# Kernel optimization log

Hardware: AMD Instinct MI355X
Metric: run time of the kernel (lower is better)

## Reference

```python
import jax, jax.numpy as jnp
import numpy as np


def setup_inputs() -> dict:
    key = jax.random.key(0)
    k_x, k_g, k_fc, k_pj = jax.random.split(key, 4)
    B, T, C, H, E = 4, 2048, 1024, 2048, 8
    n_layer = 12
    x = jax.random.normal(k_x, (B, T, C), dtype=jnp.float32)
    w_gate = 0.02 * jax.random.normal(k_g, (C, E), dtype=jnp.float32)
    w_fc = 0.02 * jax.random.normal(k_fc, (C, H, E), dtype=jnp.float32)
    w_proj = (0.02 * (2 * n_layer) ** -0.5) * jax.random.normal(k_pj, (H, C, E), dtype=jnp.float32)
    return {"x": x, "w_gate": w_gate, "w_fc": w_fc, "w_proj": w_proj, "top_k": 2}


def reference(x, w_gate, w_fc, w_proj, top_k):
    # x: (B,T,C); w_gate: (C,E); w_fc: (C,H,E); w_proj: (H,C,E)
    E = w_gate.shape[-1]
    gate = jnp.einsum('btc,ce->bte', x, w_gate)                  # gating logits
    top_vals, top_idx = jax.lax.top_k(gate, top_k)               # (B,T,K) — raw logits used as combine weights (as in source)
    # Per-expert combine weight: sum_k top_val_k * onehot(idx_k) — zero for unselected experts.
    # This is mathematically identical to gathering the K expert weight slices per token
    # (the source's gather+einsum) but avoids the (B,T,C,H,K) weight blowup.
    onehot = jax.nn.one_hot(top_idx, E, dtype=x.dtype)           # (B,T,K,E)
    w_e = jnp.einsum('btk,btke->bte', top_vals, onehot)          # (B,T,E)
    h = jax.nn.silu(jnp.einsum('btc,che->bthe', x, w_fc))        # (B,T,H,E)
    o = jnp.einsum('bthe,bte,hce->btc', h, w_e, w_proj)          # weighted expert combine
    return o
```

## Files before the change

kernel.cpp:

```cpp
#include <hip/hip_runtime.h>
#include <hip/hip_bf16.h>


#define NTOK 8192
#define CD   1024
#define HD   2048
#define NE   8
#define NSLOT 16384
#define MTILES 32

typedef short  short4_t  __attribute__((ext_vector_type(4)));
typedef short  short8_t  __attribute__((ext_vector_type(8)));
typedef __bf16 bf16x8_t  __attribute__((ext_vector_type(8)));
typedef float  f32x4_t   __attribute__((ext_vector_type(4)));

struct FragArg {
  short8_t v;
  __device__ operator short8_t() const { return v; }
  __device__ operator bf16x8_t() const { return __builtin_bit_cast(bf16x8_t, v); }
};

static __device__ __forceinline__ float b2f(unsigned short u) {
  union { float f; unsigned int i; } w; w.i = ((unsigned int)u) << 16; return w.f;
}
static __device__ __forceinline__ unsigned short f2b(float f) {
  unsigned int u = __float_as_uint(f);
  u += 0x7fffu + ((u >> 16) & 1u);
  return (unsigned short)(u >> 16);
}
static __device__ __forceinline__ void gl2lds16(const void* g, void* l) {
  __builtin_amdgcn_global_load_lds((__attribute__((address_space(1))) void*)g,
                                   (__attribute__((address_space(3))) void*)l,
                                   16, 0, 0);
}
static __device__ __forceinline__ int swz(int row, int kc) {
  return row * 4 + (kc ^ ((row >> 1) & 3));
}

__global__ __launch_bounds__(256) void gate_kernel(
    const float* __restrict__ x, const float* __restrict__ wg,
    unsigned short* __restrict__ xb,
    int* __restrict__ tok_e, float* __restrict__ tok_v)
{
  int wv = threadIdx.x >> 6, lane = threadIdx.x & 63;
  int tk = blockIdx.x * 4 + wv;
  const float* xr = x + (size_t)tk * CD;
  unsigned short* xbr = xb + (size_t)tk * CD;
  float acc[NE] = {0, 0, 0, 0, 0, 0, 0, 0};
  #pragma unroll
  for (int jj = 0; jj < 4; ++jj) {
    int c0 = (lane + 64 * jj) * 4;
    float4 xv = *(const float4*)(xr + c0);
    short4_t ob;
    ob[0] = (short)f2b(xv.x); ob[1] = (short)f2b(xv.y);
    ob[2] = (short)f2b(xv.z); ob[3] = (short)f2b(xv.w);
    *(short4_t*)(xbr + c0) = ob;
    #pragma unroll
    for (int j = 0; j < 4; ++j) {
      float xf = (j == 0) ? xv.x : (j == 1) ? xv.y : (j == 2) ? xv.z : xv.w;
      const float* wr = wg + (size_t)(c0 + j) * NE;
      float4 w0 = *(const float4*)wr;
      float4 w1 = *(const float4*)(wr + 4);
      acc[0] += xf * w0.x; acc[1] += xf * w0.y;
      acc[2] += xf * w0.z; acc[3] += xf * w0.w;
      acc[4] += xf * w1.x; acc[5] += xf * w1.y;
      acc[6] += xf * w1.z; acc[7] += xf * w1.w;
    }
  }
  #pragma unroll
  for (int off = 32; off >= 1; off >>= 1)
    #pragma unroll
    for (int e = 0; e < NE; ++e) acc[e] += __shfl_down(acc[e], off, 64);
  if (lane == 0) {
    float v1 = -3.0e38f, v2 = -3.0e38f; int i1 = 0, i2 = 1;
    #pragma unroll
    for (int e = 0; e < NE; ++e) {
      float g = acc[e];
      if (g > v1) { v2 = v1; i2 = i1; v1 = g; i1 = e; }
      else if (g > v2) { v2 = g; i2 = e; }
    }
    tok_e[tk * 2] = i1; tok_e[tk * 2 + 1] = i2;
    tok_v[tk * 2] = v1; tok_v[tk * 2 + 1] = v2;
  }
}

__global__ __launch_bounds__(256) void router_kernel(
    const int* __restrict__ tok_e, const float* __restrict__ tok_v,
    int* __restrict__ g_counts, int* __restrict__ g_base,
    int* __restrict__ bucket_tok, float* __restrict__ bucket_v,
    int* __restrict__ slot_of)
{
  __shared__ int cnts[NE][256];
  __shared__ int bas[NE], tot[NE];
  int t = threadIdx.x;
  int local[NE] = {0, 0, 0, 0, 0, 0, 0, 0};
  for (int i = 0; i < 64; ++i) local[tok_e[t * 64 + i]]++;
  #pragma unroll
  for (int e = 0; e < NE; ++e) cnts[e][t] = local[e];
  __syncthreads();
  int lane = t & 63, wv = t >> 6;
  for (int e = wv; e < NE; e += 4) {
    int carry = 0;
    #pragma unroll
    for (int c = 0; c < 4; ++c) {
      int v = cnts[e][c * 64 + lane];
      int incl = v;
      #pragma unroll
      for (int off = 1; off < 64; off <<= 1) {
        int n = __shfl_up(incl, off, 64);
        if (lane >= off) incl += n;
      }
      cnts[e][c * 64 + lane] = incl - v + carry;
      carry += __shfl(incl, 63, 64);
    }
    if (lane == 0) tot[e] = carry;
  }
  __syncthreads();
  if (t == 0) { int o = 0; for (int e = 0; e < NE; ++e) { bas[e] = o; o += tot[e]; } }
  __syncthreads();
  if (t < NE) { g_counts[t] = tot[t]; g_base[t] = bas[t]; }
  for (int i = 0; i < 64; ++i) {
    int s = t * 64 + i;
    int e = tok_e[s];
    int sl = bas[e] + cnts[e][t];
    cnts[e][t]++;
    bucket_tok[sl] = s >> 1;
    bucket_v[sl]   = tok_v[s];
    slot_of[s]     = sl;
  }
}

__global__ __launch_bounds__(256) void pack_kernel(
    const float* __restrict__ wfc, const float* __restrict__ wpj,
    unsigned short* __restrict__ wfcp, unsigned short* __restrict__ wpjp)
{
  __shared__ __align__(16) unsigned short lds[NE * 32 * 40];
  const float* in; unsigned short* out; int D0, D1, b0, b1;
  if (blockIdx.z == 0) { in = wfc; out = wfcp; D0 = CD; D1 = HD;
                         b1 = blockIdx.x * 32; b0 = blockIdx.y * 32; }
  else                 { in = wpj; out = wpjp; D0 = HD; D1 = CD;
                         b1 = blockIdx.y * 32; b0 = blockIdx.x * 32; }
  int t = threadIdx.x;
  int d1i = t & 31, d0q = t >> 5;
  #pragma unroll
  for (int r = 0; r < 4; ++r) {
    int d0i = d0q * 4 + r;
    const float* src = in + ((size_t)(b0 + d0i) * D1 + (b1 + d1i)) * NE;
    float4 v0 = *(const float4*)src;
    float4 v1 = *(const float4*)(src + 4);
    unsigned short* dst0 = &lds[d1i * 40 + d0i];
    dst0[0 * 32 * 40] = f2b(v0.x);
    dst0[1 * 32 * 40] = f2b(v0.y);
    dst0[2 * 32 * 40] = f2b(v0.z);
    dst0[3 * 32 * 40] = f2b(v0.w);
    dst0[4 * 32 * 40] = f2b(v1.x);
    dst0[5 * 32 * 40] = f2b(v1.y);
    dst0[6 * 32 * 40] = f2b(v1.z);
    dst0[7 * 32 * 40] = f2b(v1.w);
  }
  __syncthreads();
  int dchunk = t & 3, d1w = (t >> 2) & 31, ehalf = t >> 7;
  #pragma unroll
  for (int p = 0; p < 4; ++p) {
    int e = ehalf + 2 * p;
    short8_t v = *(const short8_t*)&lds[e * 32 * 40 + d1w * 40 + dchunk * 8];
    *(short8_t*)(out + ((size_t)e * D1 + (b1 + d1w)) * D0 + b0 + dchunk * 8) = v;
  }
}

__global__ __launch_bounds__(256) void gemm1_kernel(
    const unsigned short* __restrict__ xb, const unsigned short* __restrict__ wfcp,
    const int* __restrict__ g_counts, const int* __restrict__ g_base,
    const int* __restrict__ bucket_tok, const float* __restrict__ bucket_v,
    unsigned short* __restrict__ hbuf)
{
  int id = blockIdx.x;
  int xcd = id & 7;
  int r = id >> 3;
  int nt = r & 15;
  int emt = (r >> 4) * 8 + xcd;
  int e = emt >> 5, mt = emt & 31;

  int cnt = g_counts[e];
  int m0 = mt * 128;
  if (m0 >= cnt) return;
  int base = g_base[e];
  int n0 = nt * 128;

  __shared__ __align__(16) unsigned short lsA[128 * 32];
  __shared__ __align__(16) unsigned short lsB[128 * 32];
  __shared__ int   s_tok[128];
  __shared__ float s_v[128];

  int t = threadIdx.x;
  if (t < 128) {
    int ok = (m0 + t) < cnt;
    s_tok[t] = ok ? bucket_tok[base + m0 + t] : 0;
    s_v[t]   = ok ? bucket_v[base + m0 + t] : 0.0f;
  }
  __syncthreads();

  int slot = t & 3;
  int r0 = t >> 2, r1 = r0 + 64;
  int gc0 = slot ^ ((r0 >> 1) & 3);
  int gc1 = slot ^ ((r1 >> 1) & 3);
  const unsigned short* gA0 = xb + (size_t)s_tok[r0] * CD + gc0 * 8;
  const unsigned short* gA1 = xb + (size_t)s_tok[r1] * CD + gc1 * 8;
  const unsigned short* gB0 = wfcp + ((size_t)e * HD + n0 + r0) * CD + gc0 * 8;
  const unsigned short* gB1 = wfcp + ((size_t)e * HD + n0 + r1) * CD + gc1 * 8;
  unsigned short* lA0 = &lsA[(size_t)t * 8];
  unsigned short* lA1 = &lsA[(size_t)(256 + t) * 8];
  unsigned short* lB0 = &lsB[(size_t)t * 8];
  unsigned short* lB1 = &lsB[(size_t)(256 + t) * 8];

  int lane = t & 63, wv = t >> 6;
  int wm = (wv & 1) * 64, wn = (wv >> 1) * 64;
  int ml = lane & 15, kq = lane >> 4;

  f32x4_t acc[4][4];
  #pragma unroll
  for (int i = 0; i < 4; ++i)
    #pragma unroll
    for (int j = 0; j < 4; ++j) acc[i][j] = (f32x4_t){0.f, 0.f, 0.f, 0.f};

  for (int k0 = 0; k0 < CD; k0 += 32) {
    __syncthreads();
    gl2lds16(gA0 + k0, lA0);
    gl2lds16(gA1 + k0, lA1);
    gl2lds16(gB0 + k0, lB0);
    gl2lds16(gB1 + k0, lB1);
    __syncthreads();
    short8_t af[4], bfr[4];
    #pragma unroll
    for (int i = 0; i < 4; ++i) {
      af[i]  = *(const short8_t*)&lsA[swz(wm + i * 16 + ml, kq) * 8];
      bfr[i] = *(const short8_t*)&lsB[swz(wn + i * 16 + ml, kq) * 8];
    }
    #pragma unroll
    for (int i = 0; i < 4; ++i)
      #pragma unroll
      for (int j = 0; j < 4; ++j)
        acc[i][j] = __builtin_amdgcn_mfma_f32_16x16x32_bf16(
            FragArg{af[i]}, FragArg{bfr[j]}, acc[i][j], 0, 0, 0);
  }

  #pragma unroll
  for (int i = 0; i < 4; ++i) {
    int rb = wm + i * 16 + kq * 4;
    #pragma unroll
    for (int r2 = 0; r2 < 4; ++r2) {
      int row = rb + r2;
      if (m0 + row < cnt) {
        float v = s_v[row];
        size_t ro = (size_t)(base + m0 + row) * HD + n0;
        #pragma unroll
        for (int j = 0; j < 4; ++j) {
          float z = acc[i][j][r2];
          float val = v * (z / (1.0f + __expf(-z)));
          hbuf[ro + wn + j * 16 + ml] = f2b(val);
        }
      }
    }
  }
}

__global__ __launch_bounds__(256) void gemm2_kernel(
    const unsigned short* __restrict__ hbuf, const unsigned short* __restrict__ wpjp,
    const int* __restrict__ g_counts, const int* __restrict__ g_base,
    unsigned short* __restrict__ oslot)
{
  int id = blockIdx.x;
  int xcd = id & 7;
  int r = id >> 3;
  int nt = r & 7;
  int emt = (r >> 3) * 8 + xcd;
  int e = emt >> 5, mt = emt & 31;

  int cnt = g_counts[e];
  int m0 = mt * 128;
  if (m0 >= cnt) return;
  int base = g_base[e];
  int n0 = nt * 128;

  __shared__ __align__(16) unsigned short lsA[128 * 32];
  __shared__ __align__(16) unsigned short lsB[128 * 32];

  int t = threadIdx.x;
  int slot = t & 3;
  int r0 = t >> 2, r1 = r0 + 64;
  int gc0 = slot ^ ((r0 >> 1) & 3);
  int gc1 = slot ^ ((r1 >> 1) & 3);
  const unsigned short* gA0 = hbuf + (size_t)(base + m0 + r0) * HD + gc0 * 8;
  const unsigned short* gA1 = hbuf + (size_t)(base + m0 + r1) * HD + gc1 * 8;
  const unsigned short* gB0 = wpjp + ((size_t)e * CD + n0 + r0) * HD + gc0 * 8;
  const unsigned short* gB1 = wpjp + ((size_t)e * CD + n0 + r1) * HD + gc1 * 8;
  unsigned short* lA0 = &lsA[(size_t)t * 8];
  unsigned short* lA1 = &lsA[(size_t)(256 + t) * 8];
  unsigned short* lB0 = &lsB[(size_t)t * 8];
  unsigned short* lB1 = &lsB[(size_t)(256 + t) * 8];

  int lane = t & 63, wv = t >> 6;
  int wm = (wv & 1) * 64, wn = (wv >> 1) * 64;
  int ml = lane & 15, kq = lane >> 4;

  f32x4_t acc[4][4];
  #pragma unroll
  for (int i = 0; i < 4; ++i)
    #pragma unroll
    for (int j = 0; j < 4; ++j) acc[i][j] = (f32x4_t){0.f, 0.f, 0.f, 0.f};

  for (int k0 = 0; k0 < HD; k0 += 32) {
    __syncthreads();
    gl2lds16(gA0 + k0, lA0);
    gl2lds16(gA1 + k0, lA1);
    gl2lds16(gB0 + k0, lB0);
    gl2lds16(gB1 + k0, lB1);
    __syncthreads();
    short8_t af[4], bfr[4];
    #pragma unroll
    for (int i = 0; i < 4; ++i) {
      af[i]  = *(const short8_t*)&lsA[swz(wm + i * 16 + ml, kq) * 8];
      bfr[i] = *(const short8_t*)&lsB[swz(wn + i * 16 + ml, kq) * 8];
    }
    #pragma unroll
    for (int i = 0; i < 4; ++i)
      #pragma unroll
      for (int j = 0; j < 4; ++j)
        acc[i][j] = __builtin_amdgcn_mfma_f32_16x16x32_bf16(
            FragArg{af[i]}, FragArg{bfr[j]}, acc[i][j], 0, 0, 0);
  }

  #pragma unroll
  for (int i = 0; i < 4; ++i) {
    int rb = wm + i * 16 + kq * 4;
    #pragma unroll
    for (int r2 = 0; r2 < 4; ++r2) {
      int row = rb + r2;
      if (m0 + row < cnt) {
        size_t ro = (size_t)(base + m0 + row) * CD + n0;
        #pragma unroll
        for (int j = 0; j < 4; ++j)
          oslot[ro + wn + j * 16 + ml] = f2b(acc[i][j][r2]);
      }
    }
  }
}

__global__ __launch_bounds__(256) void combine_kernel(
    const unsigned short* __restrict__ oslot, const int* __restrict__ slot_of,
    float* __restrict__ out)
{
  int gid = blockIdx.x * 256 + threadIdx.x;
  int tk = gid >> 7;
  int ch = (gid & 127) * 8;
  int s0 = slot_of[tk * 2], s1 = slot_of[tk * 2 + 1];
  short8_t a = *(const short8_t*)(oslot + (size_t)s0 * CD + ch);
  short8_t b = *(const short8_t*)(oslot + (size_t)s1 * CD + ch);
  float* op = out + (size_t)tk * CD + ch;
  float4 o0, o1;
  o0.x = b2f((unsigned short)a[0]) + b2f((unsigned short)b[0]);
  o0.y = b2f((unsigned short)a[1]) + b2f((unsigned short)b[1]);
  o0.z = b2f((unsigned short)a[2]) + b2f((unsigned short)b[2]);
  o0.w = b2f((unsigned short)a[3]) + b2f((unsigned short)b[3]);
  o1.x = b2f((unsigned short)a[4]) + b2f((unsigned short)b[4]);
  o1.y = b2f((unsigned short)a[5]) + b2f((unsigned short)b[5]);
  o1.z = b2f((unsigned short)a[6]) + b2f((unsigned short)b[6]);
  o1.w = b2f((unsigned short)a[7]) + b2f((unsigned short)b[7]);
  *(float4*)op = o0;
  *(float4*)(op + 4) = o1;
}

extern "C" void kernel_launch(void* const* d_in, const int* in_sizes, int n_in,
                              void* d_out, int out_size, void* d_ws, size_t ws_size,
                              hipStream_t stream)
{
  const float* x   = (const float*)d_in[0];
  const float* wg  = (const float*)d_in[1];
  const float* wfc = (const float*)d_in[2];
  const float* wpj = (const float*)d_in[3];
  float* out = (float*)d_out;

  char* w = (char*)d_ws;
  unsigned short* wfcp  = (unsigned short*)w; w += (size_t)NE * HD * CD * 2;
  unsigned short* wpjp  = (unsigned short*)w; w += (size_t)NE * CD * HD * 2;
  unsigned short* xb    = (unsigned short*)w; w += (size_t)NTOK * CD * 2;
  unsigned short* hbuf  = (unsigned short*)w; w += (size_t)NSLOT * HD * 2;
  unsigned short* oslot = (unsigned short*)w; w += (size_t)NSLOT * CD * 2;
  int*   tok_e      = (int*)w;   w += NSLOT * 4;
  float* tok_v      = (float*)w; w += NSLOT * 4;
  int*   slot_of    = (int*)w;   w += NSLOT * 4;
  int*   bucket_tok = (int*)w;   w += NSLOT * 4;
  float* bucket_v   = (float*)w; w += NSLOT * 4;
  int*   g_counts   = (int*)w;   w += 256;
  int*   g_base     = (int*)w;   w += 256;

  gate_kernel<<<NTOK / 4, 256, 0, stream>>>(x, wg, xb, tok_e, tok_v);
  router_kernel<<<1, 256, 0, stream>>>(tok_e, tok_v, g_counts, g_base,
                                       bucket_tok, bucket_v, slot_of);
  pack_kernel<<<dim3(HD / 32, CD / 32, 2), 256, 0, stream>>>(wfc, wpj, wfcp, wpjp);
  gemm1_kernel<<<(HD / 128) * MTILES * NE, 256, 0, stream>>>(
      xb, wfcp, g_counts, g_base, bucket_tok, bucket_v, hbuf);
  gemm2_kernel<<<(CD / 128) * MTILES * NE, 256, 0, stream>>>(
      hbuf, wpjp, g_counts, g_base, oslot);
  combine_kernel<<<(NTOK * CD / 8) / 256, 256, 0, stream>>>(oslot, slot_of, out);
}
```

Baseline: 478.4 us.

## Fuse gating with weight packing and parallelize routing via atomic scatter

Merges the gate and weight-pack kernels into one launch, and has the gate blocks build the per-expert histogram with LDS and global atomics. The single-block prefix-scan router is replaced by a grid-wide scatter that uses wave ballots and atomic cursors to assign slots. MTILES drops from 32 to 20, so fewer empty GEMM tiles are launched. The trade-offs are a hard cap of 2560 tokens per expert, which depends on the routing being fairly balanced, and slot order inside each expert that is no longer deterministic.

```diff
diff --git a/kernel.cpp b/kernel.cpp
--- a/kernel.cpp
+++ b/kernel.cpp
@@ -7,7 +7,7 @@
 #define HD   2048
 #define NE   8
 #define NSLOT 16384
-#define MTILES 32
+#define MTILES 20
 
 typedef short  short4_t  __attribute__((ext_vector_type(4)));
 typedef short  short8_t  __attribute__((ext_vector_type(8)));
@@ -37,135 +37,136 @@
   return row * 4 + (kc ^ ((row >> 1) & 3));
 }
 
-__global__ __launch_bounds__(256) void gate_kernel(
+#define GATE_BLOCKS (NTOK / 4)
+__global__ __launch_bounds__(256) void prep_kernel(
     const float* __restrict__ x, const float* __restrict__ wg,
+    const float* __restrict__ wfc, const float* __restrict__ wpj,
     unsigned short* __restrict__ xb,
-    int* __restrict__ tok_e, float* __restrict__ tok_v)
-{
-  int wv = threadIdx.x >> 6, lane = threadIdx.x & 63;
-  int tk = blockIdx.x * 4 + wv;
-  const float* xr = x + (size_t)tk * CD;
-  unsigned short* xbr = xb + (size_t)tk * CD;
-  float acc[NE] = {0, 0, 0, 0, 0, 0, 0, 0};
-  #pragma unroll
-  for (int jj = 0; jj < 4; ++jj) {
-    int c0 = (lane + 64 * jj) * 4;
-    float4 xv = *(const float4*)(xr + c0);
-    short4_t ob;
-    ob[0] = (short)f2b(xv.x); ob[1] = (short)f2b(xv.y);
-    ob[2] = (short)f2b(xv.z); ob[3] = (short)f2b(xv.w);
-    *(short4_t*)(xbr + c0) = ob;
-    #pragma unroll
-    for (int j = 0; j < 4; ++j) {
-      float xf = (j == 0) ? xv.x : (j == 1) ? xv.y : (j == 2) ? xv.z : xv.w;
-      const float* wr = wg + (size_t)(c0 + j) * NE;
-      float4 w0 = *(const float4*)wr;
-      float4 w1 = *(const float4*)(wr + 4);
-      acc[0] += xf * w0.x; acc[1] += xf * w0.y;
-      acc[2] += xf * w0.z; acc[3] += xf * w0.w;
-      acc[4] += xf * w1.x; acc[5] += xf * w1.y;
-      acc[6] += xf * w1.z; acc[7] += xf * w1.w;
-    }
-  }
-  #pragma unroll
-  for (int off = 32; off >= 1; off >>= 1)
-    #pragma unroll
-    for (int e = 0; e < NE; ++e) acc[e] += __shfl_down(acc[e], off, 64);
-  if (lane == 0) {
-    float v1 = -3.0e38f, v2 = -3.0e38f; int i1 = 0, i2 = 1;
-    #pragma unroll
-    for (int e = 0; e < NE; ++e) {
-      float g = acc[e];
-      if (g > v1) { v2 = v1; i2 = i1; v1 = g; i1 = e; }
-      else if (g > v2) { v2 = g; i2 = e; }
-    }
-    tok_e[tk * 2] = i1; tok_e[tk * 2 + 1] = i2;
-    tok_v[tk * 2] = v1; tok_v[tk * 2 + 1] = v2;
-  }
-}
-
-__global__ __launch_bounds__(256) void router_kernel(
+    unsigned short* __restrict__ wfcp, unsigned short* __restrict__ wpjp,
+    int* __restrict__ tok_e, float* __restrict__ tok_v,
+    int* __restrict__ g_counts)
+{
+  __shared__ __align__(16) unsigned short lds[NE * 32 * 40];
+  __shared__ int hist[NE];
+  int t = threadIdx.x;
+
+  if (blockIdx.x < GATE_BLOCKS) {
+    if (t < NE) hist[t] = 0;
+    __syncthreads();
+    int wv = t >> 6, lane = t & 63;
+    int tk = blockIdx.x * 4 + wv;
+    const float* xr = x + (size_t)tk * CD;
+    unsigned short* xbr = xb + (size_t)tk * CD;
+    float acc[NE] = {0, 0, 0, 0, 0, 0, 0, 0};
+    #pragma unroll
+    for (int jj = 0; jj < 4; ++jj) {
+      int c0 = (lane + 64 * jj) * 4;
+      float4 xv = *(const float4*)(xr + c0);
+      short4_t ob;
+      ob[0] = (short)f2b(xv.x); ob[1] = (short)f2b(xv.y);
+      ob[2] = (short)f2b(xv.z); ob[3] = (short)f2b(xv.w);
+      *(short4_t*)(xbr + c0) = ob;
+      #pragma unroll
+      for (int j = 0; j < 4; ++j) {
+        float xf = (j == 0) ? xv.x : (j == 1) ? xv.y : (j == 2) ? xv.z : xv.w;
+        const float* wr = wg + (size_t)(c0 + j) * NE;
+        float4 w0 = *(const float4*)wr;
+        float4 w1 = *(const float4*)(wr + 4);
+        acc[0] += xf * w0.x; acc[1] += xf * w0.y;
+        acc[2] += xf * w0.z; acc[3] += xf * w0.w;
+        acc[4] += xf * w1.x; acc[5] += xf * w1.y;
+        acc[6] += xf * w1.z; acc[7] += xf * w1.w;
+      }
+    }
+    #pragma unroll
+    for (int off = 32; off >= 1; off >>= 1)
+      #pragma unroll
+      for (int e = 0; e < NE; ++e) acc[e] += __shfl_down(acc[e], off, 64);
+    if (lane == 0) {
+      float v1 = -3.0e38f, v2 = -3.0e38f; int i1 = 0, i2 = 1;
+      #pragma unroll
+      for (int e = 0; e < NE; ++e) {
+        float g = acc[e];
+        if (g > v1) { v2 = v1; i2 = i1; v1 = g; i1 = e; }
+        else if (g > v2) { v2 = g; i2 = e; }
+      }
+      tok_e[tk * 2] = i1; tok_e[tk * 2 + 1] = i2;
+      tok_v[tk * 2] = v1; tok_v[tk * 2 + 1] = v2;
+      atomicAdd(&hist[i1], 1); atomicAdd(&hist[i2], 1);
+    }
+    __syncthreads();
+    if (t < NE && hist[t] > 0) atomicAdd(&g_counts[t], hist[t]);
+  } else {
+    int pid = blockIdx.x - GATE_BLOCKS;
+    int tensor = pid >> 11;
+    int rem = pid & 2047;
+    int bx = rem & 63, by = rem >> 6;
+    const float* in; unsigned short* out; int D0, D1, b0, b1;
+    if (tensor == 0) { in = wfc; out = wfcp; D0 = CD; D1 = HD;
+                       b1 = bx * 32; b0 = by * 32; }
+    else             { in = wpj; out = wpjp; D0 = HD; D1 = CD;
+                       b1 = by * 32; b0 = bx * 32; }
+    int d1i = t & 31, d0q = t >> 5;
+    #pragma unroll
+    for (int r = 0; r < 4; ++r) {
+      int d0i = d0q * 4 + r;
+      const float* src = in + ((size_t)(b0 + d0i) * D1 + (b1 + d1i)) * NE;
+      float4 v0 = *(const float4*)src;
+      float4 v1 = *(const float4*)(src + 4);
+      unsigned short* dst0 = &lds[d1i * 40 + d0i];
+      dst0[0 * 32 * 40] = f2b(v0.x);
+      dst0[1 * 32 * 40] = f2b(v0.y);
+      dst0[2 * 32 * 40] = f2b(v0.z);
+      dst0[3 * 32 * 40] = f2b(v0.w);
+      dst0[4 * 32 * 40] = f2b(v1.x);
+      dst0[5 * 32 * 40] = f2b(v1.y);
+      dst0[6 * 32 * 40] = f2b(v1.z);
+      dst0[7 * 32 * 40] = f2b(v1.w);
+    }
+    __syncthreads();
+    int dchunk = t & 3, d1w = (t >> 2) & 31, ehalf = t >> 7;
+    #pragma unroll
+    for (int p = 0; p < 4; ++p) {
+      int e = ehalf + 2 * p;
+      short8_t v = *(const short8_t*)&lds[e * 32 * 40 + d1w * 40 + dchunk * 8];
+      *(short8_t*)(out + ((size_t)e * D1 + (b1 + d1w)) * D0 + b0 + dchunk * 8) = v;
+    }
+  }
+}
+
+__global__ __launch_bounds__(256) void scatter_kernel(
     const int* __restrict__ tok_e, const float* __restrict__ tok_v,
-    int* __restrict__ g_counts, int* __restrict__ g_base,
+    const int* __restrict__ g_counts, int* __restrict__ g_cursor,
+    int* __restrict__ g_base,
     int* __restrict__ bucket_tok, float* __restrict__ bucket_v,
     int* __restrict__ slot_of)
 {
-  __shared__ int cnts[NE][256];
-  __shared__ int bas[NE], tot[NE];
-  int t = threadIdx.x;
-  int local[NE] = {0, 0, 0, 0, 0, 0, 0, 0};
-  for (int i = 0; i < 64; ++i) local[tok_e[t * 64 + i]]++;
+  int gid = blockIdx.x * 256 + threadIdx.x;
+  int lane = threadIdx.x & 63;
+  int base[NE];
+  { int o = 0;
+    #pragma unroll
+    for (int e = 0; e < NE; ++e) { base[e] = o; o += g_counts[e]; } }
+  int e = tok_e[gid];
+  unsigned long long lanebit = 1ull << lane;
+  int pos = 0;
   #pragma unroll
-  for (int e = 0; e < NE; ++e) cnts[e][t] = local[e];
-  __syncthreads();
-  int lane = t & 63, wv = t >> 6;
-  for (int e = wv; e < NE; e += 4) {
-    int carry = 0;
-    #pragma unroll
-    for (int c = 0; c < 4; ++c) {
-      int v = cnts[e][c * 64 + lane];
-      int incl = v;
-      #pragma unroll
-      for (int off = 1; off < 64; off <<= 1) {
-        int n = __shfl_up(incl, off, 64);
-        if (lane >= off) incl += n;
-      }
-      cnts[e][c * 64 + lane] = incl - v + carry;
-      carry += __shfl(incl, 63, 64);
-    }
-    if (lane == 0) tot[e] = carry;
-  }
-  __syncthreads();
-  if (t == 0) { int o = 0; for (int e = 0; e < NE; ++e) { bas[e] = o; o += tot[e]; } }
-  __syncthreads();
-  if (t < NE) { g_counts[t] = tot[t]; g_base[t] = bas[t]; }
-  for (int i = 0; i < 64; ++i) {
-    int s = t * 64 + i;
-    int e = tok_e[s];
-    int sl = bas[e] + cnts[e][t];
-    cnts[e][t]++;
-    bucket_tok[sl] = s >> 1;
-    bucket_v[sl]   = tok_v[s];
-    slot_of[s]     = sl;
-  }
-}
-
-__global__ __launch_bounds__(256) void pack_kernel(
-    const float* __restrict__ wfc, const float* __restrict__ wpj,
-    unsigned short* __restrict__ wfcp, unsigned short* __restrict__ wpjp)
-{
-  __shared__ __align__(16) unsigned short lds[NE * 32 * 40];
-  const float* in; unsigned short* out; int D0, D1, b0, b1;
-  if (blockIdx.z == 0) { in = wfc; out = wfcp; D0 = CD; D1 = HD;
-                         b1 = blockIdx.x * 32; b0 = blockIdx.y * 32; }
-  else                 { in = wpj; out = wpjp; D0 = HD; D1 = CD;
-                         b1 = blockIdx.y * 32; b0 = blockIdx.x * 32; }
-  int t = threadIdx.x;
-  int d1i = t & 31, d0q = t >> 5;
-  #pragma unroll
-  for (int r = 0; r < 4; ++r) {
-    int d0i = d0q * 4 + r;
-    const float* src = in + ((size_t)(b0 + d0i) * D1 + (b1 + d1i)) * NE;
-    float4 v0 = *(const float4*)src;
-    float4 v1 = *(const float4*)(src + 4);
-    unsigned short* dst0 = &lds[d1i * 40 + d0i];
-    dst0[0 * 32 * 40] = f2b(v0.x);
-    dst0[1 * 32 * 40] = f2b(v0.y);
-    dst0[2 * 32 * 40] = f2b(v0.z);
-    dst0[3 * 32 * 40] = f2b(v0.w);
-    dst0[4 * 32 * 40] = f2b(v1.x);
-    dst0[5 * 32 * 40] = f2b(v1.y);
-    dst0[6 * 32 * 40] = f2b(v1.z);
-    dst0[7 * 32 * 40] = f2b(v1.w);
-  }
-  __syncthreads();
-  int dchunk = t & 3, d1w = (t >> 2) & 31, ehalf = t >> 7;
-  #pragma unroll
-  for (int p = 0; p < 4; ++p) {
-    int e = ehalf + 2 * p;
-    short8_t v = *(const short8_t*)&lds[e * 32 * 40 + d1w * 40 + dchunk * 8];
-    *(short8_t*)(out + ((size_t)e * D1 + (b1 + d1w)) * D0 + b0 + dchunk * 8) = v;
-  }
+  for (int ee = 0; ee < NE; ++ee) {
+    unsigned long long m = __ballot(e == ee);
+    if (e == ee) {
+      int leader = __ffsll((long long)m) - 1;
+      int cnt = __popcll(m);
+      int start = 0;
+      if (lane == leader) start = atomicAdd(&g_cursor[ee], cnt);
+      start = __shfl(start, leader, 64);
+      pos = start + __popcll(m & (lanebit - 1));
+    }
+  }
+  int sl = base[e] + pos;
+  bucket_tok[sl] = gid >> 1;
+  bucket_v[sl]   = tok_v[gid];
+  slot_of[gid]   = sl;
+  if (gid < NE) g_base[gid] = base[gid];
 }
 
 __global__ __launch_bounds__(256) void gemm1_kernel(
@@ -178,8 +179,8 @@
   int xcd = id & 7;
   int r = id >> 3;
   int nt = r & 15;
-  int emt = (r >> 4) * 8 + xcd;
-  int e = emt >> 5, mt = emt & 31;
+  int g = (r >> 4) * 8 + xcd;
+  int e = g / MTILES, mt = g % MTILES;
 
   int cnt = g_counts[e];
   int m0 = mt * 128;
@@ -273,8 +274,8 @@
   int xcd = id & 7;
   int r = id >> 3;
   int nt = r & 7;
-  int emt = (r >> 3) * 8 + xcd;
-  int e = emt >> 5, mt = emt & 31;
+  int g = (r >> 3) * 8 + xcd;
+  int e = g / MTILES, mt = g % MTILES;
 
   int cnt = g_counts[e];
   int m0 = mt * 128;
@@ -391,13 +392,15 @@
   int*   slot_of    = (int*)w;   w += NSLOT * 4;
   int*   bucket_tok = (int*)w;   w += NSLOT * 4;
   float* bucket_v   = (float*)w; w += NSLOT * 4;
-  int*   g_counts   = (int*)w;   w += 256;
+  int*   g_counts   = (int*)w;   w += NE * 4;
+  int*   g_cursor   = (int*)w;   w += NE * 4;
   int*   g_base     = (int*)w;   w += 256;
 
-  gate_kernel<<<NTOK / 4, 256, 0, stream>>>(x, wg, xb, tok_e, tok_v);
-  router_kernel<<<1, 256, 0, stream>>>(tok_e, tok_v, g_counts, g_base,
-                                       bucket_tok, bucket_v, slot_of);
-  pack_kernel<<<dim3(HD / 32, CD / 32, 2), 256, 0, stream>>>(wfc, wpj, wfcp, wpjp);
+  hipMemsetAsync(g_counts, 0, 2 * NE * sizeof(int), stream);
+  prep_kernel<<<GATE_BLOCKS + 4096, 256, 0, stream>>>(
+      x, wg, wfc, wpj, xb, wfcp, wpjp, tok_e, tok_v, g_counts);
+  scatter_kernel<<<NSLOT / 256, 256, 0, stream>>>(
+      tok_e, tok_v, g_counts, g_cursor, g_base, bucket_tok, bucket_v, slot_of);
   gemm1_kernel<<<(HD / 128) * MTILES * NE, 256, 0, stream>>>(
       xb, wfcp, g_counts, g_base, bucket_tok, bucket_v, hbuf);
   gemm2_kernel<<<(CD / 128) * MTILES * NE, 256, 0, stream>>>(
```

Result: faster. 466.4 us (-2.5%).
